# Kernel optimization log

Hardware: AMD Instinct MI355X
Metric: run time of the kernel (lower is better)

Reference implementation:

```python
import jax, jax.numpy as jnp
import numpy as np

N, L, S, D = 8, 1024, 4096, 512
EPS = 1e-5

def layernorm(x, g, b):
    mu = jnp.mean(x, axis=-1, keepdims=True)
    var = jnp.var(x, axis=-1, keepdims=True)
    return (x - mu) * jax.lax.rsqrt(var + EPS) * g + b

def setup_inputs() -> dict:
    key = jax.random.key(0)
    ks = jax.random.split(key, 8)
    w = lambda k, shp: jax.random.normal(k, shp, dtype=jnp.float32) * 0.02
    return {
        "x": jax.random.normal(ks[0], (N, L, D), dtype=jnp.float32),
        "source": jax.random.normal(ks[1], (N, S, D), dtype=jnp.float32),
        "Wq": w(ks[2], (D, D)),
        "Wk": w(ks[3], (D, D)),
        "Wv": w(ks[4], (D, D)),
        "Wm": w(ks[5], (D, D)),
        "W1": w(ks[6], (2 * D, 2 * D)),
        "W2": w(ks[7], (2 * D, D)),
        "g1": jnp.ones((D,), jnp.float32),
        "b1": jnp.zeros((D,), jnp.float32),
        "g2": jnp.ones((D,), jnp.float32),
        "b2": jnp.zeros((D,), jnp.float32),
    }

def reference(x, source, Wq, Wk, Wv, Wm, W1, W2, g1, b1, g2, b2):
    # projections
    q = x @ Wq          # [N, L, D]
    k = source @ Wk     # [N, S, D]
    v = source @ Wv     # [N, S, D]
    # pairwise L2 distance via ||q||^2 + ||k||^2 - 2 q.k (avoids [N,L,S,D] tensor)
    q2 = jnp.sum(q * q, axis=-1)                      # [N, L]
    k2 = jnp.sum(k * k, axis=-1)                      # [N, S]
    qk = jnp.einsum('nlc,nsc->nls', q, k)             # [N, L, S]
    dist = jnp.sqrt(jnp.maximum(q2[:, :, None] + k2[:, None, :] - 2.0 * qk, 0.0))
    attn = jax.nn.softmax(dist, axis=2)               # softmax over S (note: +distance, as in source)
    message = jnp.einsum('nls,nsc->nlc', attn, v)     # [N, L, D]
    message = layernorm(message @ Wm, g1, b1)
    h = jnp.concatenate([x, message], axis=2)         # [N, L, 2D]
    message = jax.nn.relu(h @ W1) @ W2                # [N, L, D]
    message = layernorm(message, g2, b2)
    return x + message
```

## Files before the change

### kernel.cpp

```cpp
#include <hip/hip_runtime.h>
#include <stdint.h>

typedef unsigned short u16;
typedef __attribute__((ext_vector_type(8))) short bf16x8;
typedef __attribute__((ext_vector_type(4))) float f32x4;
typedef __attribute__((ext_vector_type(4))) unsigned int u32x4;

__device__ __forceinline__ u16 f2b(float f) {
  uint32_t u = __float_as_uint(f);
  u += 0x7fffu + ((u >> 16) & 1u);
  return (u16)(u >> 16);
}
__device__ __forceinline__ float b2f(u16 h) {
  return __uint_as_float(((uint32_t)h) << 16);
}
__device__ __forceinline__ uint32_t pack2bf(float a, float b) {
#if __has_builtin(__builtin_amdgcn_cvt_pk_bf16_f32)
  typedef __attribute__((ext_vector_type(2))) __bf16 bf16x2_t;
  bf16x2_t r = __builtin_amdgcn_cvt_pk_bf16_f32(a, b);
  return __builtin_bit_cast(uint32_t, r);
#else
  return (uint32_t)f2b(a) | ((uint32_t)f2b(b) << 16);
#endif
}

__device__ __forceinline__ void gload_lds16(const u16* g, u16* l) {
  __builtin_amdgcn_global_load_lds(
      (const __attribute__((address_space(1))) void*)g,
      (__attribute__((address_space(3))) void*)l, 16, 0, 0);
}

enum { EPI_BF16_T = 0, EPI_BF16_T_SQ = 1, EPI_F32_T = 2, EPI_RELU_BF16_T = 3,
       EPI_EXP_T = 4 };

template <int EPI>
__device__ __forceinline__ void gemm_body(
    u16* smem, const u16* A, size_t sA, int lda,
    const u16* B, size_t sB, int ldb,
    void* C, size_t sC, int ldc, int K, size_t pStride,
    const float* e_col2, const float* e_row2, float* e_l,
    int lin, int gx, int gy) {
  u16* As = smem;
  u16* Bs = smem + 8192;
  const int t = threadIdx.x;
  const int batch = lin & 7;
  const int rest = lin >> 3;
  const int bx = rest % gx;
  const int ry = rest / gx;
  const int by = ry % gy;
  const int part = ry / gy;
  const int m0 = by * 128, n0 = bx * 128;
  const int koff = part * K;
  const u16* Ab = A + (size_t)batch * sA + (size_t)m0 * lda + koff;
  const u16* Bb = B + (size_t)batch * sB + (size_t)n0 * ldb + koff;
  const int srow = t >> 3;
  const int skey = (srow & 3) | (((srow >> 3) & 1) << 2);
  const int scol = ((t & 7) ^ skey) << 3;
  const u16* aS = Ab + (size_t)srow * lda + scol;
  const u16* bS = Bb + (size_t)srow * ldb + scol;
  const size_t a32 = (size_t)32 * lda, b32 = (size_t)32 * ldb;
  u16* asDst = As + t * 8;
  u16* bsDst = Bs + t * 8;

  const int w = t >> 6, lane = t & 63;
  const int wm = (w >> 1) << 6, wn = (w & 1) << 6;
  const int qd = lane >> 4, l16 = lane & 15;
  const int rbase = ((l16 >> 2) << 3) + (l16 & 3);
  const int keyA = (l16 & 3) | (((l16 >> 2) & 1) << 2);
  const int keyB = (l16 & 3) | (((l16 >> 3) & 1) << 2);
  const u16* aRow0 = As + (wm + rbase) * 64;
  const u16* bRow0 = Bs + (wn + l16) * 64;

  f32x4 acc[4][4];
#pragma unroll
  for (int i = 0; i < 4; i++)
#pragma unroll
    for (int j = 0; j < 4; j++) acc[i][j] = (f32x4)0.0f;

  for (int k0 = 0; k0 < K; k0 += 64) {
    gload_lds16(aS, asDst);
    gload_lds16(aS + a32, asDst + 2048);
    gload_lds16(aS + 2 * a32, asDst + 4096);
    gload_lds16(aS + 3 * a32, asDst + 6144);
    gload_lds16(bS, bsDst);
    gload_lds16(bS + b32, bsDst + 2048);
    gload_lds16(bS + 2 * b32, bsDst + 4096);
    gload_lds16(bS + 3 * b32, bsDst + 6144);
    aS += 64;
    bS += 64;
    __syncthreads();
#pragma unroll
    for (int s = 0; s < 2; s++) {
      const int ca = (((qd | (s << 2)) ^ keyA) << 3);
      const int cb = (((qd | (s << 2)) ^ keyB) << 3);
      bf16x8 af[4], bfr[4];
      af[0] = *(const bf16x8*)(aRow0 + ca);
      af[1] = *(const bf16x8*)(aRow0 + 4 * 64 + ca);
      af[2] = *(const bf16x8*)(aRow0 + 32 * 64 + ca);
      af[3] = *(const bf16x8*)(aRow0 + 36 * 64 + ca);
#pragma unroll
      for (int i = 0; i < 4; i++)
        bfr[i] = *(const bf16x8*)(bRow0 + i * 16 * 64 + cb);
#pragma unroll
      for (int mi = 0; mi < 4; mi++)
#pragma unroll
        for (int ni = 0; ni < 4; ni++)
          acc[mi][ni] = __builtin_amdgcn_mfma_f32_16x16x32_bf16(
              af[mi], bfr[ni], acc[mi][ni], 0, 0, 0);
    }
    __syncthreads();
  }

  const size_t cbase = (size_t)part * pStride + (size_t)batch * sC;
  const int ncols = (int)(sC / ldc);

  if constexpr (EPI == EPI_EXP_T) {
    const int nrows = (int)(sA / lda);
    const float* col2 = e_col2 + (size_t)batch * ncols;
    const float* row2 = e_row2 + (size_t)batch * nrows;
    float* lb = e_l + (size_t)batch * ncols;
    float c2v[4];
#pragma unroll
    for (int ni = 0; ni < 4; ni++) c2v[ni] = col2[n0 + wn + ni * 16 + l16];
    float cs[4] = {0.f, 0.f, 0.f, 0.f};
#pragma unroll
    for (int p = 0; p < 2; p++) {
      const int prow = m0 + wm + p * 32 + qd * 8;
      float r2v[8];
#pragma unroll
      for (int r8 = 0; r8 < 8; r8++) r2v[r8] = row2[prow + r8];
#pragma unroll
      for (int ni = 0; ni < 4; ni++) {
        const int col = n0 + wn + ni * 16 + l16;
        float pv[8];
#pragma unroll
        for (int r = 0; r < 4; r++) {
          pv[r] = __expf(sqrtf(
              fmaxf(c2v[ni] + r2v[r] - 2.0f * acc[2 * p][ni][r], 0.0f)));
          pv[4 + r] = __expf(sqrtf(
              fmaxf(c2v[ni] + r2v[4 + r] - 2.0f * acc[2 * p + 1][ni][r], 0.0f)));
        }
#pragma unroll
        for (int j = 0; j < 8; j++) cs[ni] += pv[j];
        u32x4 wv;
        wv[0] = pack2bf(pv[0], pv[1]);
        wv[1] = pack2bf(pv[2], pv[3]);
        wv[2] = pack2bf(pv[4], pv[5]);
        wv[3] = pack2bf(pv[6], pv[7]);
        *(u32x4*)((u16*)C + cbase + (size_t)col * ldc + prow) = wv;
      }
    }
#pragma unroll
    for (int ni = 0; ni < 4; ni++) {
      cs[ni] += __shfl_xor(cs[ni], 16);
      cs[ni] += __shfl_xor(cs[ni], 32);
    }
    if (qd == 0) {
#pragma unroll
      for (int ni = 0; ni < 4; ni++)
        atomicAdd(lb + n0 + wn + ni * 16 + l16, cs[ni]);
    }
  } else if constexpr (EPI == EPI_F32_T) {
#pragma unroll
    for (int p = 0; p < 2; p++) {
      const int prow = m0 + wm + p * 32 + qd * 8;
#pragma unroll
      for (int ni = 0; ni < 4; ni++) {
        const int col = n0 + wn + ni * 16 + l16;
        float* dst = (float*)C + cbase + (size_t)col * ldc + prow;
        *(f32x4*)dst = acc[2 * p][ni];
        *(f32x4*)(dst + 4) = acc[2 * p + 1][ni];
      }
    }
  } else {
    float cs[4] = {0.f, 0.f, 0.f, 0.f};
#pragma unroll
    for (int p = 0; p < 2; p++) {
      const int prow = m0 + wm + p * 32 + qd * 8;
#pragma unroll
      for (int ni = 0; ni < 4; ni++) {
        const int col = n0 + wn + ni * 16 + l16;
        float v[8];
#pragma unroll
        for (int r = 0; r < 4; r++) {
          v[r] = acc[2 * p][ni][r];
          v[4 + r] = acc[2 * p + 1][ni][r];
        }
        if (EPI == EPI_RELU_BF16_T) {
#pragma unroll
          for (int j = 0; j < 8; j++) v[j] = fmaxf(v[j], 0.0f);
        }
        if (EPI == EPI_BF16_T_SQ) {
#pragma unroll
          for (int j = 0; j < 8; j++) cs[ni] += v[j] * v[j];
        }
        u32x4 wv;
        wv[0] = pack2bf(v[0], v[1]);
        wv[1] = pack2bf(v[2], v[3]);
        wv[2] = pack2bf(v[4], v[5]);
        wv[3] = pack2bf(v[6], v[7]);
        *(u32x4*)((u16*)C + cbase + (size_t)col * ldc + prow) = wv;
      }
    }
    if (EPI == EPI_BF16_T_SQ) {
#pragma unroll
      for (int ni = 0; ni < 4; ni++) {
        cs[ni] += __shfl_xor(cs[ni], 16);
        cs[ni] += __shfl_xor(cs[ni], 32);
      }
      if (qd == 0) {
#pragma unroll
        for (int ni = 0; ni < 4; ni++)
          atomicAdd(e_l + (size_t)batch * ncols + n0 + wn + ni * 16 + l16,
                    cs[ni]);
      }
    }
  }
}

template <int EPI>
__global__ __launch_bounds__(256, 2) void gemm_nt(
    const u16* __restrict__ A, size_t sA, int lda,
    const u16* __restrict__ B, size_t sB, int ldb,
    void* __restrict__ C, size_t sC, int ldc, int K, size_t pStride,
    const float* __restrict__ e_col2, const float* __restrict__ e_row2,
    float* __restrict__ e_l) {
  __shared__ __align__(16) u16 smem[16384];
  const int lin = blockIdx.x + gridDim.x * (blockIdx.y + gridDim.y * blockIdx.z);
  gemm_body<EPI>(smem, A, sA, lda, B, sB, ldb, C, sC, ldc, K, pStride,
                 e_col2, e_row2, e_l, lin, gridDim.x, gridDim.y);
}

__global__ __launch_bounds__(256, 2) void proj_fused(
    const u16* __restrict__ WqT, const u16* __restrict__ WkT,
    const u16* __restrict__ WvT, const u16* __restrict__ h,
    const u16* __restrict__ sb, u16* __restrict__ q, u16* __restrict__ kb,
    u16* __restrict__ vT, float* __restrict__ q2, float* __restrict__ k2) {
  __shared__ __align__(16) u16 smem[16384];
  const int lin = blockIdx.x;
  if (lin < 256) {
    gemm_body<EPI_BF16_T_SQ>(smem, WqT, 0, 512, h, (size_t)1024 * 1024, 1024,
                             q, (size_t)1024 * 512, 512, 512, 0, nullptr,
                             nullptr, q2, lin, 8, 4);
  } else if (lin < 1280) {
    gemm_body<EPI_BF16_T_SQ>(smem, WkT, 0, 512, sb, (size_t)4096 * 512, 512,
                             kb, (size_t)4096 * 512, 512, 512, 0, nullptr,
                             nullptr, k2, lin - 256, 32, 4);
  } else {
    gemm_body<EPI_BF16_T>(smem, sb, (size_t)4096 * 512, 512, WvT, 0, 512,
                          vT, (size_t)512 * 4096, 4096, 512, 0, nullptr,
                          nullptr, nullptr, lin - 1280, 4, 32);
  }
}

__global__ __launch_bounds__(256) void reduce2_div_bf16(
    const float* __restrict__ P, const float* __restrict__ l,
    u16* __restrict__ out) {
  const size_t i = (size_t)blockIdx.x * 256 + threadIdx.x;
  const float4* p = (const float4*)P;
  float4 a = p[i];
  float4 b = p[i + 1048576];
  const float inv = 1.0f / l[i >> 7];
  ushort4 o = make_ushort4(f2b((a.x + b.x) * inv), f2b((a.y + b.y) * inv),
                           f2b((a.z + b.z) * inv), f2b((a.w + b.w) * inv));
  *(ushort4*)(out + (i << 2)) = o;
}

__global__ __launch_bounds__(256) void fused_prep(
    const float* __restrict__ x, const float* __restrict__ sc,
    u16* __restrict__ h, u16* __restrict__ sb, float* __restrict__ q2,
    float* __restrict__ k2, float* __restrict__ lsum) {
  const size_t i = (size_t)blockIdx.x * 256 + threadIdx.x;
  if (i < 1048576) {
    const float4 f = ((const float4*)x)[i];
    const int e = (int)(i << 2);
    const int row = e >> 9, col = e & 511;
    *(ushort4*)(h + ((size_t)row << 10) + col) =
        make_ushort4(f2b(f.x), f2b(f.y), f2b(f.z), f2b(f.w));
  } else if (i < 5242880) {
    const size_t j = i - 1048576;
    const float4 f = ((const float4*)sc)[j];
    *(ushort4*)(sb + (j << 2)) =
        make_ushort4(f2b(f.x), f2b(f.y), f2b(f.z), f2b(f.w));
  } else {
    const size_t j = i - 5242880;
    const float4 z = {0.f, 0.f, 0.f, 0.f};
    if (j < 2048) ((float4*)q2)[j] = z;
    else if (j < 10240) ((float4*)k2)[j - 2048] = z;
    else ((float4*)lsum)[j - 10240] = z;
  }
}

__global__ void transpose_w6(
    const float* __restrict__ Wq, const float* __restrict__ Wk,
    const float* __restrict__ Wv, const float* __restrict__ Wm,
    const float* __restrict__ W1, const float* __restrict__ W2,
    u16* __restrict__ WqT, u16* __restrict__ WkT, u16* __restrict__ WvT,
    u16* __restrict__ WmT, u16* __restrict__ W1T, u16* __restrict__ W2T) {
  __shared__ float tile[32][33];
  const float* W;
  u16* WT;
  int R, Cn;
  switch (blockIdx.z) {
    case 0: W = Wq; WT = WqT; R = 512; Cn = 512; break;
    case 1: W = Wk; WT = WkT; R = 512; Cn = 512; break;
    case 2: W = Wv; WT = WvT; R = 512; Cn = 512; break;
    case 3: W = Wm; WT = WmT; R = 512; Cn = 512; break;
    case 4: W = W1; WT = W1T; R = 1024; Cn = 1024; break;
    default: W = W2; WT = W2T; R = 1024; Cn = 512; break;
  }
  const int c0 = blockIdx.x * 32, r0 = blockIdx.y * 32;
  if (c0 >= Cn || r0 >= R) return;
  const int tx = threadIdx.x, ty = threadIdx.y;
  for (int i = ty; i < 32; i += 8) tile[i][tx] = W[(size_t)(r0 + i) * Cn + c0 + tx];
  __syncthreads();
  for (int i = ty; i < 32; i += 8) WT[(size_t)(c0 + i) * R + r0 + tx] = f2b(tile[tx][i]);
}

__global__ __launch_bounds__(128) void ln_to_h(const float* __restrict__ mm,
                                               const float* __restrict__ g,
                                               const float* __restrict__ b,
                                               u16* __restrict__ h) {
  const size_t row = blockIdx.x;
  const int t = threadIdx.x;
  const float4 f = ((const float4*)(mm + row * 512))[t];
  float s = f.x + f.y + f.z + f.w;
  float sq = f.x * f.x + f.y * f.y + f.z * f.z + f.w * f.w;
#pragma unroll
  for (int off = 32; off; off >>= 1) { s += __shfl_xor(s, off); sq += __shfl_xor(sq, off); }
  __shared__ float rs_[2], rq_[2];
  if ((t & 63) == 0) { rs_[t >> 6] = s; rq_[t >> 6] = sq; }
  __syncthreads();
  s = rs_[0] + rs_[1]; sq = rq_[0] + rq_[1];
  const float mu = s * (1.0f / 512.0f);
  const float rstd = rsqrtf(sq * (1.0f / 512.0f) - mu * mu + 1e-5f);
  const float4 gv = ((const float4*)g)[t], bv = ((const float4*)b)[t];
  ushort4 o = make_ushort4(f2b((f.x - mu) * rstd * gv.x + bv.x),
                           f2b((f.y - mu) * rstd * gv.y + bv.y),
                           f2b((f.z - mu) * rstd * gv.z + bv.z),
                           f2b((f.w - mu) * rstd * gv.w + bv.w));
  *(ushort4*)(h + (row << 10) + 512 + (t << 2)) = o;
}

__global__ __launch_bounds__(128) void ln_residual(const float* __restrict__ m2,
                                                   const float* __restrict__ x,
                                                   const float* __restrict__ g,
                                                   const float* __restrict__ b,
                                                   float* __restrict__ out) {
  const size_t row = blockIdx.x;
  const int t = threadIdx.x;
  const float4 f = ((const float4*)(m2 + row * 512))[t];
  float s = f.x + f.y + f.z + f.w;
  float sq = f.x * f.x + f.y * f.y + f.z * f.z + f.w * f.w;
#pragma unroll
  for (int off = 32; off; off >>= 1) { s += __shfl_xor(s, off); sq += __shfl_xor(sq, off); }
  __shared__ float rs_[2], rq_[2];
  if ((t & 63) == 0) { rs_[t >> 6] = s; rq_[t >> 6] = sq; }
  __syncthreads();
  s = rs_[0] + rs_[1]; sq = rq_[0] + rq_[1];
  const float mu = s * (1.0f / 512.0f);
  const float rstd = rsqrtf(sq * (1.0f / 512.0f) - mu * mu + 1e-5f);
  const float4 gv = ((const float4*)g)[t], bv = ((const float4*)b)[t];
  const float4 xv = ((const float4*)(x + row * 512))[t];
  float4 o;
  o.x = xv.x + (f.x - mu) * rstd * gv.x + bv.x;
  o.y = xv.y + (f.y - mu) * rstd * gv.y + bv.y;
  o.z = xv.z + (f.z - mu) * rstd * gv.z + bv.z;
  o.w = xv.w + (f.w - mu) * rstd * gv.w + bv.w;
  ((float4*)(out + row * 512))[t] = o;
}

extern "C" void kernel_launch(void* const* d_in, const int* in_sizes, int n_in,
                              void* d_out, int out_size, void* d_ws, size_t ws_size,
                              hipStream_t stream) {
  const float* x  = (const float*)d_in[0];
  const float* sc = (const float*)d_in[1];
  const float* Wq = (const float*)d_in[2];
  const float* Wk = (const float*)d_in[3];
  const float* Wv = (const float*)d_in[4];
  const float* Wm = (const float*)d_in[5];
  const float* W1 = (const float*)d_in[6];
  const float* W2 = (const float*)d_in[7];
  const float* g1 = (const float*)d_in[8];
  const float* b1 = (const float*)d_in[9];
  const float* g2 = (const float*)d_in[10];
  const float* b2 = (const float*)d_in[11];
  float* out = (float*)d_out;
  char* ws = (char*)d_ws;

  constexpr int N = 8, L = 1024, S = 4096, D = 512;
  u16*   h   = (u16*)(ws + 0);
  u16*   sb  = (u16*)(ws + 16777216);
  u16*   WqT = (u16*)(ws + 50331648);
  u16*   WkT = (u16*)(ws + 50855936);
  u16*   WvT = (u16*)(ws + 51380224);
  u16*   WmT = (u16*)(ws + 51904512);
  u16*   W1T = (u16*)(ws + 52428800);
  u16*   W2T = (u16*)(ws + 54525952);
  u16*   q   = (u16*)(ws + 55574528);
  u16*   kb  = (u16*)(ws + 63963136);
  u16*   vT  = (u16*)(ws + 97517568);
  float* lsum= (float*)(ws + 131072000);
  float* q2  = (float*)(ws + 164626432);
  float* k2  = (float*)(ws + 164659200);
  u16*   qk  = (u16*)(ws + 164790272);
  u16*   msg = (u16*)(ws + 55574528);
  float* mpart = (float*)(ws + 63963136);
  float* mm  = (float*)(ws + 63963136);
  u16*   hh  = (u16*)(ws + 80740352);
  float* m2  = (float*)(ws + 97517568);

  fused_prep<<<dim3(20528), 256, 0, stream>>>(x, sc, h, sb, q2, k2, lsum);
  transpose_w6<<<dim3(32, 32, 6), dim3(32, 8), 0, stream>>>(
      Wq, Wk, Wv, Wm, W1, W2, WqT, WkT, WvT, WmT, W1T, W2T);

  proj_fused<<<dim3(2304), 256, 0, stream>>>(WqT, WkT, WvT, h, sb, q, kb, vT,
                                             q2, k2);

  gemm_nt<EPI_EXP_T><<<dim3(8, 32, 8), 256, 0, stream>>>(
      kb, (size_t)S * 512, 512, q, (size_t)L * 512, 512, qk, (size_t)L * S, S,
      512, 0, q2, k2, lsum);
  gemm_nt<EPI_F32_T><<<dim3(8, 4, 16), 256, 0, stream>>>(
      vT, (size_t)D * S, S, qk, (size_t)L * S, S, mpart, (size_t)L * 512, 512,
      2048, (size_t)(N * L) * 512, nullptr, nullptr, nullptr);
  reduce2_div_bf16<<<dim3(4096), 256, 0, stream>>>(mpart, lsum, msg);

  gemm_nt<EPI_F32_T><<<dim3(8, 4, 8), 256, 0, stream>>>(
      WmT, 0, 512, msg, (size_t)L * 512, 512, mm, (size_t)L * 512, 512, 512, 0,
      nullptr, nullptr, nullptr);
  ln_to_h<<<dim3(N * L), 128, 0, stream>>>(mm, g1, b1, h);

  gemm_nt<EPI_RELU_BF16_T><<<dim3(8, 8, 8), 256, 0, stream>>>(
      W1T, 0, 1024, h, (size_t)L * 1024, 1024, hh, (size_t)L * 1024, 1024, 1024,
      0, nullptr, nullptr, nullptr);
  gemm_nt<EPI_F32_T><<<dim3(8, 4, 8), 256, 0, stream>>>(
      W2T, 0, 1024, hh, (size_t)L * 1024, 1024, m2, (size_t)L * 512, 512, 1024,
      0, nullptr, nullptr, nullptr);

  ln_residual<<<dim3(N * L), 128, 0, stream>>>(m2, x, g2, b2, out);
}
```

Baseline: 364.4 us.

## Add 256x128 tile GEMM body for projections and distance-exp GEMM

Introduces a larger-tile GEMM body (256 rows per block, 8x4 MFMA accumulators per wave) and uses it for the Q/K/V projection kernel and the distance/exp attention-score GEMM, halving the grid sizes. The larger tiles raise arithmetic intensity and cut global/LDS reloads per output. The cost is more accumulator registers and more LDS per block (48KB), which may reduce occupancy, and the original body's epilogue branches are reshuffled.

```diff
diff --git a/kernel.cpp b/kernel.cpp
--- a/kernel.cpp
+++ b/kernel.cpp
@@ -114,6 +114,124 @@
   const size_t cbase = (size_t)part * pStride + (size_t)batch * sC;
   const int ncols = (int)(sC / ldc);
 
+  if constexpr (EPI == EPI_F32_T) {
+#pragma unroll
+    for (int p = 0; p < 2; p++) {
+      const int prow = m0 + wm + p * 32 + qd * 8;
+#pragma unroll
+      for (int ni = 0; ni < 4; ni++) {
+        const int col = n0 + wn + ni * 16 + l16;
+        float* dst = (float*)C + cbase + (size_t)col * ldc + prow;
+        *(f32x4*)dst = acc[2 * p][ni];
+        *(f32x4*)(dst + 4) = acc[2 * p + 1][ni];
+      }
+    }
+  } else {
+#pragma unroll
+    for (int p = 0; p < 2; p++) {
+      const int prow = m0 + wm + p * 32 + qd * 8;
+#pragma unroll
+      for (int ni = 0; ni < 4; ni++) {
+        const int col = n0 + wn + ni * 16 + l16;
+        float v[8];
+#pragma unroll
+        for (int r = 0; r < 4; r++) {
+          v[r] = acc[2 * p][ni][r];
+          v[4 + r] = acc[2 * p + 1][ni][r];
+        }
+        if (EPI == EPI_RELU_BF16_T) {
+#pragma unroll
+          for (int j = 0; j < 8; j++) v[j] = fmaxf(v[j], 0.0f);
+        }
+        u32x4 wv;
+        wv[0] = pack2bf(v[0], v[1]);
+        wv[1] = pack2bf(v[2], v[3]);
+        wv[2] = pack2bf(v[4], v[5]);
+        wv[3] = pack2bf(v[6], v[7]);
+        *(u32x4*)((u16*)C + cbase + (size_t)col * ldc + prow) = wv;
+      }
+    }
+  }
+}
+
+template <int EPI>
+__device__ __forceinline__ void gemm_body_big(
+    u16* smem, const u16* A, size_t sA, int lda,
+    const u16* B, size_t sB, int ldb,
+    void* C, size_t sC, int ldc, int K,
+    const float* e_col2, const float* e_row2, float* e_l,
+    int lin, int gx, int gy) {
+  u16* As = smem;
+  u16* Bs = smem + 16384;
+  const int t = threadIdx.x;
+  const int batch = lin & 7;
+  const int rest = lin >> 3;
+  const int bx = rest % gx;
+  const int by = rest / gx;
+  const int m0 = by * 256, n0 = bx * 128;
+  const u16* Ab = A + (size_t)batch * sA + (size_t)m0 * lda;
+  const u16* Bb = B + (size_t)batch * sB + (size_t)n0 * ldb;
+  const int srow = t >> 3;
+  const int skey = (srow & 3) | (((srow >> 3) & 1) << 2);
+  const int scol = ((t & 7) ^ skey) << 3;
+  const u16* aS = Ab + (size_t)srow * lda + scol;
+  const u16* bS = Bb + (size_t)srow * ldb + scol;
+  const size_t a32 = (size_t)32 * lda, b32 = (size_t)32 * ldb;
+  u16* asDst = As + t * 8;
+  u16* bsDst = Bs + t * 8;
+
+  const int w = t >> 6, lane = t & 63;
+  const int wm = (w >> 1) << 7;
+  const int wn = (w & 1) << 6;
+  const int qd = lane >> 4, l16 = lane & 15;
+  const int rbase = ((l16 >> 2) << 3) + (l16 & 3);
+  const int keyA = (l16 & 3) | (((l16 >> 2) & 1) << 2);
+  const int keyB = (l16 & 3) | (((l16 >> 3) & 1) << 2);
+  const u16* aRow0 = As + (wm + rbase) * 64;
+  const u16* bRow0 = Bs + (wn + l16) * 64;
+
+  f32x4 acc[8][4];
+#pragma unroll
+  for (int i = 0; i < 8; i++)
+#pragma unroll
+    for (int j = 0; j < 4; j++) acc[i][j] = (f32x4)0.0f;
+
+  for (int k0 = 0; k0 < K; k0 += 64) {
+#pragma unroll
+    for (int j = 0; j < 8; j++)
+      gload_lds16(aS + j * a32, asDst + j * 2048);
+#pragma unroll
+    for (int j = 0; j < 4; j++)
+      gload_lds16(bS + j * b32, bsDst + j * 2048);
+    aS += 64;
+    bS += 64;
+    __syncthreads();
+#pragma unroll
+    for (int s = 0; s < 2; s++) {
+      const int ca = (((qd | (s << 2)) ^ keyA) << 3);
+      const int cb = (((qd | (s << 2)) ^ keyB) << 3);
+      bf16x8 af[8], bfr[4];
+#pragma unroll
+      for (int g = 0; g < 4; g++) {
+        af[2 * g] = *(const bf16x8*)(aRow0 + (32 * g) * 64 + ca);
+        af[2 * g + 1] = *(const bf16x8*)(aRow0 + (32 * g + 4) * 64 + ca);
+      }
+#pragma unroll
+      for (int i = 0; i < 4; i++)
+        bfr[i] = *(const bf16x8*)(bRow0 + i * 16 * 64 + cb);
+#pragma unroll
+      for (int mi = 0; mi < 8; mi++)
+#pragma unroll
+        for (int ni = 0; ni < 4; ni++)
+          acc[mi][ni] = __builtin_amdgcn_mfma_f32_16x16x32_bf16(
+              af[mi], bfr[ni], acc[mi][ni], 0, 0, 0);
+    }
+    __syncthreads();
+  }
+
+  const size_t cbase = (size_t)batch * sC;
+  const int ncols = (int)(sC / ldc);
+
   if constexpr (EPI == EPI_EXP_T) {
     const int nrows = (int)(sA / lda);
     const float* col2 = e_col2 + (size_t)batch * ncols;
@@ -124,8 +242,8 @@
     for (int ni = 0; ni < 4; ni++) c2v[ni] = col2[n0 + wn + ni * 16 + l16];
     float cs[4] = {0.f, 0.f, 0.f, 0.f};
 #pragma unroll
-    for (int p = 0; p < 2; p++) {
-      const int prow = m0 + wm + p * 32 + qd * 8;
+    for (int g = 0; g < 4; g++) {
+      const int prow = m0 + wm + 32 * g + qd * 8;
       float r2v[8];
 #pragma unroll
       for (int r8 = 0; r8 < 8; r8++) r2v[r8] = row2[prow + r8];
@@ -136,9 +254,9 @@
 #pragma unroll
         for (int r = 0; r < 4; r++) {
           pv[r] = __expf(sqrtf(
-              fmaxf(c2v[ni] + r2v[r] - 2.0f * acc[2 * p][ni][r], 0.0f)));
+              fmaxf(c2v[ni] + r2v[r] - 2.0f * acc[2 * g][ni][r], 0.0f)));
           pv[4 + r] = __expf(sqrtf(
-              fmaxf(c2v[ni] + r2v[4 + r] - 2.0f * acc[2 * p + 1][ni][r], 0.0f)));
+              fmaxf(c2v[ni] + r2v[4 + r] - 2.0f * acc[2 * g + 1][ni][r], 0.0f)));
         }
 #pragma unroll
         for (int j = 0; j < 8; j++) cs[ni] += pv[j];
@@ -160,35 +278,19 @@
       for (int ni = 0; ni < 4; ni++)
         atomicAdd(lb + n0 + wn + ni * 16 + l16, cs[ni]);
     }
-  } else if constexpr (EPI == EPI_F32_T) {
-#pragma unroll
-    for (int p = 0; p < 2; p++) {
-      const int prow = m0 + wm + p * 32 + qd * 8;
-#pragma unroll
-      for (int ni = 0; ni < 4; ni++) {
-        const int col = n0 + wn + ni * 16 + l16;
-        float* dst = (float*)C + cbase + (size_t)col * ldc + prow;
-        *(f32x4*)dst = acc[2 * p][ni];
-        *(f32x4*)(dst + 4) = acc[2 * p + 1][ni];
-      }
-    }
   } else {
     float cs[4] = {0.f, 0.f, 0.f, 0.f};
 #pragma unroll
-    for (int p = 0; p < 2; p++) {
-      const int prow = m0 + wm + p * 32 + qd * 8;
+    for (int g = 0; g < 4; g++) {
+      const int prow = m0 + wm + 32 * g + qd * 8;
 #pragma unroll
       for (int ni = 0; ni < 4; ni++) {
         const int col = n0 + wn + ni * 16 + l16;
         float v[8];
 #pragma unroll
         for (int r = 0; r < 4; r++) {
-          v[r] = acc[2 * p][ni][r];
-          v[4 + r] = acc[2 * p + 1][ni][r];
-        }
-        if (EPI == EPI_RELU_BF16_T) {
-#pragma unroll
-          for (int j = 0; j < 8; j++) v[j] = fmaxf(v[j], 0.0f);
+          v[r] = acc[2 * g][ni][r];
+          v[4 + r] = acc[2 * g + 1][ni][r];
         }
         if (EPI == EPI_BF16_T_SQ) {
 #pragma unroll
@@ -231,25 +333,38 @@
                  e_col2, e_row2, e_l, lin, gridDim.x, gridDim.y);
 }
 
+template <int EPI>
+__global__ __launch_bounds__(256, 2) void gemm_nt_big(
+    const u16* __restrict__ A, size_t sA, int lda,
+    const u16* __restrict__ B, size_t sB, int ldb,
+    void* __restrict__ C, size_t sC, int ldc, int K,
+    const float* __restrict__ e_col2, const float* __restrict__ e_row2,
+    float* __restrict__ e_l) {
+  __shared__ __align__(16) u16 smem[24576];
+  const int lin = blockIdx.x + gridDim.x * (blockIdx.y + gridDim.y * blockIdx.z);
+  gemm_body_big<EPI>(smem, A, sA, lda, B, sB, ldb, C, sC, ldc, K,
+                     e_col2, e_row2, e_l, lin, gridDim.x, gridDim.y);
+}
+
 __global__ __launch_bounds__(256, 2) void proj_fused(
     const u16* __restrict__ WqT, const u16* __restrict__ WkT,
     const u16* __restrict__ WvT, const u16* __restrict__ h,
     const u16* __restrict__ sb, u16* __restrict__ q, u16* __restrict__ kb,
     u16* __restrict__ vT, float* __restrict__ q2, float* __restrict__ k2) {
-  __shared__ __align__(16) u16 smem[16384];
+  __shared__ __align__(16) u16 smem[24576];
   const int lin = blockIdx.x;
-  if (lin < 256) {
-    gemm_body<EPI_BF16_T_SQ>(smem, WqT, 0, 512, h, (size_t)1024 * 1024, 1024,
-                             q, (size_t)1024 * 512, 512, 512, 0, nullptr,
-                             nullptr, q2, lin, 8, 4);
-  } else if (lin < 1280) {
-    gemm_body<EPI_BF16_T_SQ>(smem, WkT, 0, 512, sb, (size_t)4096 * 512, 512,
-                             kb, (size_t)4096 * 512, 512, 512, 0, nullptr,
-                             nullptr, k2, lin - 256, 32, 4);
+  if (lin < 128) {
+    gemm_body_big<EPI_BF16_T_SQ>(smem, WqT, 0, 512, h, (size_t)1024 * 1024,
+                                 1024, q, (size_t)1024 * 512, 512, 512,
+                                 nullptr, nullptr, q2, lin, 8, 2);
+  } else if (lin < 640) {
+    gemm_body_big<EPI_BF16_T_SQ>(smem, WkT, 0, 512, sb, (size_t)4096 * 512,
+                                 512, kb, (size_t)4096 * 512, 512, 512,
+                                 nullptr, nullptr, k2, lin - 128, 32, 2);
   } else {
-    gemm_body<EPI_BF16_T>(smem, sb, (size_t)4096 * 512, 512, WvT, 0, 512,
-                          vT, (size_t)512 * 4096, 4096, 512, 0, nullptr,
-                          nullptr, nullptr, lin - 1280, 4, 32);
+    gemm_body_big<EPI_BF16_T>(smem, sb, (size_t)4096 * 512, 512, WvT, 0, 512,
+                              vT, (size_t)512 * 4096, 4096, 512, nullptr,
+                              nullptr, nullptr, lin - 640, 4, 16);
   }
 }
 
@@ -414,12 +529,12 @@
   transpose_w6<<<dim3(32, 32, 6), dim3(32, 8), 0, stream>>>(
       Wq, Wk, Wv, Wm, W1, W2, WqT, WkT, WvT, WmT, W1T, W2T);
 
-  proj_fused<<<dim3(2304), 256, 0, stream>>>(WqT, WkT, WvT, h, sb, q, kb, vT,
+  proj_fused<<<dim3(1152), 256, 0, stream>>>(WqT, WkT, WvT, h, sb, q, kb, vT,
                                              q2, k2);
 
-  gemm_nt<EPI_EXP_T><<<dim3(8, 32, 8), 256, 0, stream>>>(
+  gemm_nt_big<EPI_EXP_T><<<dim3(8, 16, 8), 256, 0, stream>>>(
       kb, (size_t)S * 512, 512, q, (size_t)L * 512, 512, qk, (size_t)L * S, S,
-      512, 0, q2, k2, lsum);
+      512, q2, k2, lsum);
   gemm_nt<EPI_F32_T><<<dim3(8, 4, 16), 256, 0, stream>>>(
       vT, (size_t)D * S, S, qk, (size_t)L * S, S, mpart, (size_t)L * 512, 512,
       2048, (size_t)(N * L) * 512, nullptr, nullptr, nullptr);
```

After: 382.9 us. 5.1% more time.
